# Performance work log

Hardware: AMD Instinct MI355X
Metric: run time of the kernel (lower is better)

Reference implementation:

```python
import jax, jax.numpy as jnp
import numpy as np

NMUL = 1
NEARZERO = 1e-5
ROUTING_LEN = 15
N_DYN = 3
N_STATIC = 13  # layout includes parRT, parAC (present in STATIC_PARAM_NAMES but unused in the step)


def _descale(x, lb, ub):
    return lb + x * (ub - lb)


def setup_inputs() -> dict:
    key = jax.random.key(0)
    k1, k2, k3 = jax.random.split(key, 3)
    T, G = 365, 50000
    u = jax.random.uniform(k1, (T, G, 3), dtype=jnp.float32)
    prcp = u[..., 0] * 10.0                 # mm/day
    tmean = (u[..., 1] - 0.3) * 20.0        # degC, roughly [-6, 14] so snow branch is exercised
    pet = u[..., 2] * 5.0                   # mm/day
    forcing = jnp.stack([prcp, tmean, pet], axis=-1)
    dyn_raw = jax.random.uniform(k2, (T, G, N_DYN * NMUL), dtype=jnp.float32)
    static_raw = jax.random.uniform(k3, (G, N_STATIC * NMUL + 2), dtype=jnp.float32)
    return {"forcing": forcing, "dyn_raw": dyn_raw, "static_raw": static_raw}


def _hbv_forward(forcing, dyn_raw, static_raw):
    T, G, _ = forcing.shape
    dt = forcing.dtype
    # --- descale dynamic params (per-timestep): parBETA, parK0, parBETAET ---
    dyn = dyn_raw.reshape(T, G, N_DYN, NMUL)
    parBETA = _descale(dyn[:, :, 0], 1.0, 6.0)
    parK0 = _descale(dyn[:, :, 1], 0.05, 0.9)
    parBETAET = _descale(dyn[:, :, 2], 0.3, 5.0)
    # --- descale static params ---
    st = static_raw[:, :N_STATIC * NMUL].reshape(G, N_STATIC, NMUL)
    parFC = _descale(st[:, 0], 50.0, 1000.0)
    parK1 = _descale(st[:, 1], 0.01, 0.5)
    parK2 = _descale(st[:, 2], 0.001, 0.2)
    parLP = _descale(st[:, 3], 0.2, 1.0)
    parPERC = _descale(st[:, 4], 0.0, 10.0)
    parUZL = _descale(st[:, 5], 0.0, 100.0)
    parTT = _descale(st[:, 6], -2.5, 2.5)
    parCFMAX = _descale(st[:, 7], 0.5, 10.0)
    parCFR = _descale(st[:, 8], 0.0, 0.1)
    parCWH = _descale(st[:, 9], 0.0, 0.2)
    parC = _descale(st[:, 10], 0.0, 1.0)
    rout = static_raw[:, N_STATIC * NMUL:]
    rout_a = _descale(rout[:, 0], 0.0, 2.9)
    rout_b = _descale(rout[:, 1], 0.0, 6.5)

    Pm = jnp.broadcast_to(forcing[..., 0:1], (T, G, NMUL))
    Tm = jnp.broadcast_to(forcing[..., 1:2], (T, G, NMUL))
    PETm = jnp.broadcast_to(forcing[..., 2:3], (T, G, NMUL))

    def step(carry, xs):
        SNOWPACK, MELTWATER, SM, SUZ, SLZ = carry
        PRECIP, TEMP, PET, pBETA, pK0, pBETAET = xs
        is_rain = (TEMP >= parTT).astype(dt)
        RAIN = PRECIP * is_rain
        SNOW = PRECIP * (1.0 - is_rain)
        SNOWPACK = SNOWPACK + SNOW
        melt = jnp.minimum(jnp.maximum(parCFMAX * (TEMP - parTT), 0.0), SNOWPACK)
        MELTWATER = MELTWATER + melt
        SNOWPACK = SNOWPACK - melt
        refreezing = jnp.minimum(jnp.maximum(parCFR * parCFMAX * (parTT - TEMP), 0.0), MELTWATER)
        SNOWPACK = SNOWPACK + refreezing
        MELTWATER = MELTWATER - refreezing
        tosoil = jnp.maximum(MELTWATER - parCWH * SNOWPACK, 0.0)
        MELTWATER = MELTWATER - tosoil
        soil_wetness = jnp.clip((SM / parFC) ** pBETA, 0.0, 1.0)
        recharge = (RAIN + tosoil) * soil_wetness
        SM = SM + RAIN + tosoil - recharge
        excess = jnp.maximum(SM - parFC, 0.0)
        SM = SM - excess
        evapfactor = jnp.clip((SM / (parLP * parFC)) ** pBETAET, 0.0, 1.0)
        ETact = jnp.minimum(SM, PET * evapfactor)
        SM = jnp.maximum(SM - ETact, NEARZERO)
        capillary = jnp.minimum(SLZ, parC * SLZ * (1.0 - jnp.minimum(SM / parFC, 1.0)))
        SM = jnp.maximum(SM + capillary, NEARZERO)
        SLZ = jnp.maximum(SLZ - capillary, NEARZERO)
        SUZ = SUZ + recharge + excess
        PERC = jnp.minimum(SUZ, parPERC)
        SUZ = SUZ - PERC
        Q0 = pK0 * jnp.maximum(SUZ - parUZL, 0.0)
        SUZ = SUZ - Q0
        Q1 = parK1 * SUZ
        SUZ = SUZ - Q1
        SLZ = jnp.maximum(SLZ + PERC, 0.0)
        Q2 = parK2 * SLZ
        SLZ = SLZ - Q2
        return (SNOWPACK, MELTWATER, SM, SUZ, SLZ), Q0 + Q1 + Q2

    init = tuple(jnp.full((G, NMUL), 0.001, dtype=dt) for _ in range(5))
    _, Qall = jax.lax.scan(step, init, (Pm, Tm, PETm, parBETA, parK0, parBETAET))
    Qsim = Qall.mean(axis=-1)  # [T, G]: average over nmul components

    # --- gamma unit-hydrograph routing (hydroDL UH_gamma + causal conv, lenF = 15) ---
    aa = jax.nn.relu(rout_a) + 0.1      # shape param, [G]
    theta = jax.nn.relu(rout_b) + 0.5   # scale param, [G]
    t = jnp.arange(0.5, ROUTING_LEN, dtype=dt)[:, None]  # [15, 1] midpoints
    w = (t ** (aa - 1.0)) * jnp.exp(-t / theta) / (jnp.exp(jax.lax.lgamma(aa)) * theta ** aa)
    w = w / w.sum(axis=0)  # [15, G], normalized UH weights
    Qpad = jnp.pad(Qsim, ((ROUTING_LEN - 1, 0), (0, 0)))
    # causal conv: Qrout[t] = sum_k w[k] * Qsim[t-k]; fixed 15-tap loop
    Qrout = sum(w[k] * jax.lax.dynamic_slice_in_dim(Qpad, ROUTING_LEN - 1 - k, T, axis=0)
                for k in range(ROUTING_LEN))
    return Qrout  # streamflow [T, G]


def reference(forcing, dyn_raw, static_raw):
    return _hbv_forward(forcing, dyn_raw, static_raw)
```

## Files before the change

kernel.cpp:

```cpp
#include <hip/hip_runtime.h>

#define NEARZERO 1e-5f
#define RLEN 15
#define LOG2E 1.4426950408889634f

struct __attribute__((packed, aligned(4))) F3 { float x, y, z; };
static __device__ __forceinline__ F3 ld3f(const float* p) {
    return *reinterpret_cast<const F3*>(p);
}

struct Par { float FC, invFC, invLPFC, K1, K2, PERC, UZL, TT, CFMAX, CFRC, CWH, C; };

template<int PH>
__device__ __forceinline__ float one_step(
    const F3& f, const F3& d3, const Par& pr,
    float& SNOWPACK, float& MELTWATER, float& SM, float& SUZ, float& SLZ,
    float (&acc)[RLEN], const float (&w)[RLEN])
{
    const float pBETA   = fmaf(d3.x, 5.0f, 1.0f);
    const float pK0     = fmaf(d3.y, 0.85f, 0.05f);
    const float pBETAET = fmaf(d3.z, 4.7f, 0.3f);

    const float d    = f.y - pr.TT;
    const float RAIN = (d >= 0.0f) ? f.x : 0.0f;
    SNOWPACK += f.x - RAIN;
    const float melt = __builtin_amdgcn_fmed3f(pr.CFMAX * d, 0.0f, SNOWPACK);
    MELTWATER += melt;
    SNOWPACK  -= melt;
    const float refr = __builtin_amdgcn_fmed3f(pr.CFRC * (0.0f - d), 0.0f, MELTWATER);
    SNOWPACK  += refr;
    MELTWATER -= refr;
    const float tosoil = fmaxf(fmaf(-pr.CWH, SNOWPACK, MELTWATER), 0.0f);
    MELTWATER -= tosoil;

    const float sw = fminf(exp2f(pBETA * __log2f(SM * pr.invFC)), 1.0f);
    const float rt = RAIN + tosoil;
    const float recharge = rt * sw;
    SM = SM + rt - recharge;
    const float excess = fmaxf(SM - pr.FC, 0.0f);
    SM -= excess;
    const float ef = fminf(exp2f(pBETAET * __log2f(SM * pr.invLPFC)), 1.0f);
    const float ETact = fminf(SM, f.z * ef);
    SM = fmaxf(SM - ETact, NEARZERO);
    const float capillary = pr.C * SLZ * (1.0f - fminf(SM * pr.invFC, 1.0f));
    SM  = fmaxf(SM + capillary, NEARZERO);
    SLZ = fmaxf(SLZ - capillary, NEARZERO);

    SUZ += recharge + excess;
    const float PERC = fminf(SUZ, pr.PERC);
    SUZ -= PERC;
    const float Q0 = pK0 * fmaxf(SUZ - pr.UZL, 0.0f);
    SUZ -= Q0;
    const float Q1 = pr.K1 * SUZ;
    SUZ -= Q1;
    SLZ += PERC;
    const float Q2 = pr.K2 * SLZ;
    SLZ -= Q2;
    const float Qsim = Q0 + Q1 + Q2;

    const float qr = fmaf(w[0], Qsim, acc[PH]);
    acc[PH] = 0.0f;
#pragma unroll
    for (int k = 1; k < RLEN; ++k) {
        const int j = (PH + k) % RLEN;
        acc[j] = fmaf(w[k], Qsim, acc[j]);
    }
    return qr;
}

__global__ __launch_bounds__(64, 1)
void hbv_kernel(const float* __restrict__ forcing,
                const float* __restrict__ dynr,
                const float* __restrict__ statr,
                float* __restrict__ out,
                int G)
{
    const int lane = threadIdx.x;
    const int g  = blockIdx.x * 64 + lane;
    const int gc = (g < G) ? g : (G - 1);
    const bool guard = (g < G);

    const float* sp = statr + (size_t)gc * 15;
    Par pr;
    pr.FC    = fmaf(sp[0], 950.0f, 50.0f);
    pr.K1    = fmaf(sp[1], 0.49f, 0.01f);
    pr.K2    = fmaf(sp[2], 0.199f, 0.001f);
    const float parLP = fmaf(sp[3], 0.8f, 0.2f);
    pr.PERC  = sp[4] * 10.0f;
    pr.UZL   = sp[5] * 100.0f;
    pr.TT    = fmaf(sp[6], 5.0f, -2.5f);
    pr.CFMAX = fmaf(sp[7], 9.5f, 0.5f);
    pr.CFRC  = (sp[8] * 0.1f) * pr.CFMAX;
    pr.CWH   = sp[9] * 0.2f;
    pr.C     = sp[10];
    const float rout_a = sp[13] * 2.9f;
    const float rout_b = sp[14] * 6.5f;
    pr.invFC   = 1.0f / pr.FC;
    pr.invLPFC = 1.0f / (parLP * pr.FC);

    const float aa    = fmaxf(rout_a, 0.0f) + 0.1f;
    const float theta = fmaxf(rout_b, 0.0f) + 0.5f;
    const float am1   = aa - 1.0f;
    const float nitl2 = -LOG2E / theta;
    float w[RLEN];
    float wsum = 0.0f;
#pragma unroll
    for (int k = 0; k < RLEN; ++k) {
        const float tk = (float)k + 0.5f;
        w[k] = exp2f(am1 * __log2f(tk) + tk * nitl2);
        wsum += w[k];
    }
    const float winv = 1.0f / wsum;
#pragma unroll
    for (int k = 0; k < RLEN; ++k) w[k] *= winv;

    float SP_ = 0.001f, MW = 0.001f, SM = 0.001f, SUZ = 0.001f, SLZ = 0.001f;
    float acc[RLEN];
#pragma unroll
    for (int k = 0; k < RLEN; ++k) acc[k] = 0.0f;

    const size_t sT = (size_t)G * 3;
    const float* pF = forcing + (size_t)gc * 3;
    const float* pD = dynr    + (size_t)gc * 3;

    F3 bF[3], bD[3];
    bF[0] = ld3f(pF);          bD[0] = ld3f(pD);
    bF[1] = ld3f(pF + sT);     bD[1] = ld3f(pD + sT);
    bF[2] = ld3f(pF + 2 * sT); bD[2] = ld3f(pD + 2 * sT);

    const float* rF = pF + 3 * sT;
    const float* rD = pD + 3 * sT;
    float* outp = out + g;

#define STEP(PH, FP, DP) do { \
    constexpr int P_ = (PH) % RLEN; \
    constexpr int S_ = P_ % 3; \
    const float qr_ = one_step<P_>(bF[S_], bD[S_], pr, \
                                   SP_, MW, SM, SUZ, SLZ, acc, w); \
    bF[S_] = ld3f(FP); bD[S_] = ld3f(DP); \
    __builtin_amdgcn_sched_barrier(0x7); \
    if (guard) __builtin_nontemporal_store(qr_, outp); \
    outp += G; \
} while (0)

#define STEPADV(PH) do { \
    STEP(PH, rF, rD); \
    rF += sT; rD += sT; \
} while (0)

    for (int i = 0; i < 24; ++i) {
        STEPADV(0);  STEPADV(1);  STEPADV(2);  STEPADV(3);  STEPADV(4);
        STEPADV(5);  STEPADV(6);  STEPADV(7);  STEPADV(8);  STEPADV(9);
        STEPADV(10); STEPADV(11); STEPADV(12); STEPADV(13); STEPADV(14);
    }
#define TR(T) ((((T) + 3) <= 364) ? ((T) + 3) : 364)
    STEP(0, pF + (size_t)TR(360) * sT, pD + (size_t)TR(360) * sT);
    STEP(1, pF + (size_t)TR(361) * sT, pD + (size_t)TR(361) * sT);
    STEP(2, pF + (size_t)TR(362) * sT, pD + (size_t)TR(362) * sT);
    STEP(3, pF + (size_t)TR(363) * sT, pD + (size_t)TR(363) * sT);
    STEP(4, pF + (size_t)TR(364) * sT, pD + (size_t)TR(364) * sT);
#undef TR
#undef STEPADV
#undef STEP
}

extern "C" void kernel_launch(void* const* d_in, const int* in_sizes, int n_in,
                              void* d_out, int out_size, void* d_ws, size_t ws_size,
                              hipStream_t stream) {
    const float* forcing = (const float*)d_in[0];
    const float* dynr    = (const float*)d_in[1];
    const float* statr   = (const float*)d_in[2];
    float* out = (float*)d_out;

    const int G = in_sizes[2] / 15;
    const int block = 64;
    const int grid  = (G + block - 1) / block;
    hbv_kernel<<<grid, block, 0, stream>>>(forcing, dynr, statr, out, G);
}
```

Baseline: 114.1 us.

## Split HBV step into snow/soil and groundwater/routing halves, software-pipelined

Splits each timestep into a snow/soil phase and a groundwater/routing phase. The soil phase for step t+1 is issued right after the routing phase of step t, and capillary flow uses a precomputed C*SLZ product, so the two dependency chains can overlap. The prefetch depth grows from 3 to 5 timesteps. Output stores go from nontemporal to regular stores. This adds register pressure and a more complex prologue and epilogue, and reassociating SM updates may change rounding slightly.

```diff
diff --git a/kernel.cpp b/kernel.cpp
--- a/kernel.cpp
+++ b/kernel.cpp
@@ -12,60 +12,68 @@
 struct Par { float FC, invFC, invLPFC, K1, K2, PERC, UZL, TT, CFMAX, CFRC, CWH, C; };
 
 template<int PH>
-__device__ __forceinline__ float one_step(
-    const F3& f, const F3& d3, const Par& pr,
-    float& SNOWPACK, float& MELTWATER, float& SM, float& SUZ, float& SLZ,
-    float (&acc)[RLEN], const float (&w)[RLEN])
+__device__ __forceinline__ void finish_step(
+    const Par& pr, float& SUZ, float& SLZ,
+    float rxP, float k0P,
+    float (&acc)[RLEN], const float (&w)[RLEN],
+    float& cs, float*& outp, int G, bool guard)
 {
-    const float pBETA   = fmaf(d3.x, 5.0f, 1.0f);
-    const float pK0     = fmaf(d3.y, 0.85f, 0.05f);
-    const float pBETAET = fmaf(d3.z, 4.7f, 0.3f);
-
-    const float d    = f.y - pr.TT;
-    const float RAIN = (d >= 0.0f) ? f.x : 0.0f;
-    SNOWPACK += f.x - RAIN;
-    const float melt = __builtin_amdgcn_fmed3f(pr.CFMAX * d, 0.0f, SNOWPACK);
-    MELTWATER += melt;
-    SNOWPACK  -= melt;
-    const float refr = __builtin_amdgcn_fmed3f(pr.CFRC * (0.0f - d), 0.0f, MELTWATER);
-    SNOWPACK  += refr;
-    MELTWATER -= refr;
-    const float tosoil = fmaxf(fmaf(-pr.CWH, SNOWPACK, MELTWATER), 0.0f);
-    MELTWATER -= tosoil;
-
-    const float sw = fminf(exp2f(pBETA * __log2f(SM * pr.invFC)), 1.0f);
-    const float rt = RAIN + tosoil;
-    const float recharge = rt * sw;
-    SM = SM + rt - recharge;
-    const float excess = fmaxf(SM - pr.FC, 0.0f);
-    SM -= excess;
-    const float ef = fminf(exp2f(pBETAET * __log2f(SM * pr.invLPFC)), 1.0f);
-    const float ETact = fminf(SM, f.z * ef);
-    SM = fmaxf(SM - ETact, NEARZERO);
-    const float capillary = pr.C * SLZ * (1.0f - fminf(SM * pr.invFC, 1.0f));
-    SM  = fmaxf(SM + capillary, NEARZERO);
-    SLZ = fmaxf(SLZ - capillary, NEARZERO);
-
-    SUZ += recharge + excess;
-    const float PERC = fminf(SUZ, pr.PERC);
-    SUZ -= PERC;
-    const float Q0 = pK0 * fmaxf(SUZ - pr.UZL, 0.0f);
+    SUZ += rxP;
+    const float PERCv = fminf(SUZ, pr.PERC);
+    SUZ -= PERCv;
+    const float Q0 = k0P * fmaxf(SUZ - pr.UZL, 0.0f);
     SUZ -= Q0;
     const float Q1 = pr.K1 * SUZ;
     SUZ -= Q1;
-    SLZ += PERC;
+    SLZ += PERCv;
     const float Q2 = pr.K2 * SLZ;
     SLZ -= Q2;
-    const float Qsim = Q0 + Q1 + Q2;
-
-    const float qr = fmaf(w[0], Qsim, acc[PH]);
+    const float Qs = Q0 + Q1 + Q2;
+
+    const float qr = fmaf(w[0], Qs, acc[PH]);
     acc[PH] = 0.0f;
 #pragma unroll
     for (int k = 1; k < RLEN; ++k) {
         const int j = (PH + k) % RLEN;
-        acc[j] = fmaf(w[k], Qsim, acc[j]);
-    }
-    return qr;
+        acc[j] = fmaf(w[k], Qs, acc[j]);
+    }
+    if (guard) *outp = qr;
+    outp += G;
+    cs = pr.C * SLZ;
+}
+
+__device__ __forceinline__ void ab_step(
+    const F3& f, const F3& d3, const Par& pr,
+    float& SP, float& MW, float& SM, float& SLZ,
+    float cs, float& rxP, float& k0P)
+{
+    const float pBETA   = fmaf(d3.x, 5.0f, 1.0f);
+    const float pBETAET = fmaf(d3.z, 4.7f, 0.3f);
+
+    const float dT   = f.y - pr.TT;
+    const float RAIN = (dT >= 0.0f) ? f.x : 0.0f;
+    SP += f.x - RAIN;
+    const float melt = __builtin_amdgcn_fmed3f(pr.CFMAX * dT, 0.0f, SP);
+    MW += melt;  SP -= melt;
+    const float refr = __builtin_amdgcn_fmed3f(pr.CFRC * (0.0f - dT), 0.0f, MW);
+    SP += refr;  MW -= refr;
+    const float tosoil = fmaxf(fmaf(-pr.CWH, SP, MW), 0.0f);
+    MW -= tosoil;
+
+    const float sw = fminf(exp2f(pBETA * __log2f(SM * pr.invFC)), 1.0f);
+    const float rt = RAIN + tosoil;
+    const float rc = rt * sw;
+    SM = fmaf(rt, 1.0f - sw, SM);
+    const float ex = fmaxf(SM - pr.FC, 0.0f);
+    SM = fminf(SM, pr.FC);
+    const float ef = fminf(exp2f(pBETAET * __log2f(SM * pr.invLPFC)), 1.0f);
+    SM = fmaxf(SM - f.z * ef, NEARZERO);
+    const float cap = cs * (1.0f - fminf(SM * pr.invFC, 1.0f));
+    SM  = fmaxf(SM + cap, NEARZERO);
+    SLZ = fmaxf(SLZ - cap, NEARZERO);
+
+    rxP = rc + ex;
+    k0P = fmaf(d3.y, 0.85f, 0.05f);
 }
 
 __global__ __launch_bounds__(64, 1)
@@ -118,50 +126,66 @@
     float acc[RLEN];
 #pragma unroll
     for (int k = 0; k < RLEN; ++k) acc[k] = 0.0f;
+    float rxP = 0.0f, k0P = 0.0f, cs = 0.0f;
 
     const size_t sT = (size_t)G * 3;
     const float* pF = forcing + (size_t)gc * 3;
     const float* pD = dynr    + (size_t)gc * 3;
-
-    F3 bF[3], bD[3];
+    float* outp = out + g;
+
+    F3 bF[5], bD[5];
     bF[0] = ld3f(pF);          bD[0] = ld3f(pD);
     bF[1] = ld3f(pF + sT);     bD[1] = ld3f(pD + sT);
     bF[2] = ld3f(pF + 2 * sT); bD[2] = ld3f(pD + 2 * sT);
-
-    const float* rF = pF + 3 * sT;
-    const float* rD = pD + 3 * sT;
-    float* outp = out + g;
-
-#define STEP(PH, FP, DP) do { \
-    constexpr int P_ = (PH) % RLEN; \
-    constexpr int S_ = P_ % 3; \
-    const float qr_ = one_step<P_>(bF[S_], bD[S_], pr, \
-                                   SP_, MW, SM, SUZ, SLZ, acc, w); \
+    bF[3] = ld3f(pF + 3 * sT); bD[3] = ld3f(pD + 3 * sT);
+    bF[4] = ld3f(pF + 4 * sT); bD[4] = ld3f(pD + 4 * sT);
+
+    const float* rF = pF + 5 * sT;
+    const float* rD = pD + 5 * sT;
+
+    cs = pr.C * SLZ;
+    {
+        const F3 f_ = bF[0], d_ = bD[0];
+        bF[0] = ld3f(rF); bD[0] = ld3f(rD);
+        rF += sT; rD += sT;
+        __builtin_amdgcn_sched_barrier(0x7);
+        ab_step(f_, d_, pr, SP_, MW, SM, SLZ, cs, rxP, k0P);
+    }
+
+#define ITER(MM, FP, DP) do { \
+    constexpr int PH_ = (MM) % RLEN; \
+    constexpr int S_  = ((MM) + 1) % 5; \
+    finish_step<PH_>(pr, SUZ, SLZ, rxP, k0P, acc, w, cs, outp, G, guard); \
+    const F3 f_ = bF[S_], d_ = bD[S_]; \
     bF[S_] = ld3f(FP); bD[S_] = ld3f(DP); \
     __builtin_amdgcn_sched_barrier(0x7); \
-    if (guard) __builtin_nontemporal_store(qr_, outp); \
-    outp += G; \
+    ab_step(f_, d_, pr, SP_, MW, SM, SLZ, cs, rxP, k0P); \
 } while (0)
 
-#define STEPADV(PH) do { \
-    STEP(PH, rF, rD); \
-    rF += sT; rD += sT; \
+#define ITERADV(MM) do { ITER(MM, rF, rD); rF += sT; rD += sT; } while (0)
+
+#define ITER_NL(MM) do { \
+    constexpr int PH_ = (MM) % RLEN; \
+    constexpr int S_  = ((MM) + 1) % 5; \
+    finish_step<PH_>(pr, SUZ, SLZ, rxP, k0P, acc, w, cs, outp, G, guard); \
+    const F3 f_ = bF[S_], d_ = bD[S_]; \
+    ab_step(f_, d_, pr, SP_, MW, SM, SLZ, cs, rxP, k0P); \
 } while (0)
 
-    for (int i = 0; i < 24; ++i) {
-        STEPADV(0);  STEPADV(1);  STEPADV(2);  STEPADV(3);  STEPADV(4);
-        STEPADV(5);  STEPADV(6);  STEPADV(7);  STEPADV(8);  STEPADV(9);
-        STEPADV(10); STEPADV(11); STEPADV(12); STEPADV(13); STEPADV(14);
-    }
-#define TR(T) ((((T) + 3) <= 364) ? ((T) + 3) : 364)
-    STEP(0, pF + (size_t)TR(360) * sT, pD + (size_t)TR(360) * sT);
-    STEP(1, pF + (size_t)TR(361) * sT, pD + (size_t)TR(361) * sT);
-    STEP(2, pF + (size_t)TR(362) * sT, pD + (size_t)TR(362) * sT);
-    STEP(3, pF + (size_t)TR(363) * sT, pD + (size_t)TR(363) * sT);
-    STEP(4, pF + (size_t)TR(364) * sT, pD + (size_t)TR(364) * sT);
-#undef TR
-#undef STEPADV
-#undef STEP
+    for (int i = 0; i < 23; ++i) {
+        ITERADV(0);  ITERADV(1);  ITERADV(2);  ITERADV(3);  ITERADV(4);
+        ITERADV(5);  ITERADV(6);  ITERADV(7);  ITERADV(8);  ITERADV(9);
+        ITERADV(10); ITERADV(11); ITERADV(12); ITERADV(13); ITERADV(14);
+    }
+    ITERADV(0);  ITERADV(1);  ITERADV(2);  ITERADV(3);  ITERADV(4);
+    ITERADV(5);  ITERADV(6);  ITERADV(7);  ITERADV(8);  ITERADV(9);
+    ITERADV(10); ITERADV(11); ITERADV(12); ITERADV(13);
+    ITER(14, pF + (size_t)364 * sT, pD + (size_t)364 * sT);
+    ITER_NL(0); ITER_NL(1); ITER_NL(2); ITER_NL(3);
+    finish_step<4>(pr, SUZ, SLZ, rxP, k0P, acc, w, cs, outp, G, guard);
+#undef ITER_NL
+#undef ITERADV
+#undef ITER
 }
 
 extern "C" void kernel_launch(void* const* d_in, const int* in_sizes, int n_in,
```

New measurement: 103.9 us. 1.1x faster.

## Add producer wave staging inputs to LDS ring and software-pipeline the step

Applied to the files above, without the earlier changes.

Each block now has two waves. One producer wave streams forcing and dynamic parameters into a double-buffered LDS ring ten timesteps at a time, and the consumer wave runs the recurrence from LDS, with __syncthreads handing off between them. The step is also skewed so the groundwater part of step t overlaps the log2 work of step t+1, which shortens the serial dependency chain, and global addressing moves to 32-bit byte offsets. The aim is to hide global load latency behind the serial compute, at the cost of a barrier every group, LDS traffic, and an extra wave per CU slot.

```diff
diff --git a/kernel.cpp b/kernel.cpp
--- a/kernel.cpp
+++ b/kernel.cpp
@@ -3,165 +3,266 @@
 #define NEARZERO 1e-5f
 #define RLEN 15
 #define LOG2E 1.4426950408889634f
+#define GRP 10
 
 struct __attribute__((packed, aligned(4))) F3 { float x, y, z; };
-static __device__ __forceinline__ F3 ld3f(const float* p) {
-    return *reinterpret_cast<const F3*>(p);
+static __device__ __forceinline__ F3 ldo(const char* base, unsigned voff) {
+    return *reinterpret_cast<const F3*>(base + voff);
 }
 
 struct Par { float FC, invFC, invLPFC, K1, K2, PERC, UZL, TT, CFMAX, CFRC, CWH, C; };
 
+struct CState {
+    Par pr;
+    float SP, MW, SM, SUZ, SLZ, rxP, k0P;
+    float acc[RLEN], w[RLEN];
+    char* obase;
+    unsigned vO, G4;
+    bool guard;
+};
+
+__device__ __forceinline__ void ab_step0(CState& st, const F3 f, const F3 d3)
+{
+    const Par& pr = st.pr;
+    const float cs = pr.C * st.SLZ;
+    const float dT   = f.y - pr.TT;
+    const float RAIN = (dT >= 0.0f) ? f.x : 0.0f;
+    st.SP += f.x - RAIN;
+    const float melt = __builtin_amdgcn_fmed3f(pr.CFMAX * dT, 0.0f, st.SP);
+    st.MW += melt;  st.SP -= melt;
+    const float refr = __builtin_amdgcn_fmed3f(pr.CFRC * (0.0f - dT), 0.0f, st.MW);
+    st.SP += refr;  st.MW -= refr;
+    const float tosoil = fmaxf(fmaf(-pr.CWH, st.SP, st.MW), 0.0f);
+    st.MW -= tosoil;
+    const float sw = fminf(exp2f(fmaf(d3.x, 5.0f, 1.0f) * __log2f(st.SM * pr.invFC)), 1.0f);
+    const float rt = RAIN + tosoil;
+    const float rc = rt * sw;
+    st.SM = fmaf(rt, 1.0f - sw, st.SM);
+    const float ex = fmaxf(st.SM - pr.FC, 0.0f);
+    st.SM = fminf(st.SM, pr.FC);
+    const float ef = fminf(exp2f(fmaf(d3.z, 4.7f, 0.3f) * __log2f(st.SM * pr.invLPFC)), 1.0f);
+    st.SM = fmaxf(st.SM - f.z * ef, NEARZERO);
+    const float cap = cs * (1.0f - fminf(st.SM * pr.invFC, 1.0f));
+    st.SM  = fmaxf(st.SM + cap, NEARZERO);
+    st.SLZ = fmaxf(st.SLZ - cap, NEARZERO);
+    st.rxP = rc + ex;
+    st.k0P = fmaf(d3.y, 0.85f, 0.05f);
+}
+
 template<int PH>
-__device__ __forceinline__ float one_step(
-    const F3& f, const F3& d3, const Par& pr,
-    float& SNOWPACK, float& MELTWATER, float& SM, float& SUZ, float& SLZ,
-    float (&acc)[RLEN], const float (&w)[RLEN])
-{
-    const float pBETA   = fmaf(d3.x, 5.0f, 1.0f);
-    const float pK0     = fmaf(d3.y, 0.85f, 0.05f);
-    const float pBETAET = fmaf(d3.z, 4.7f, 0.3f);
-
-    const float d    = f.y - pr.TT;
-    const float RAIN = (d >= 0.0f) ? f.x : 0.0f;
-    SNOWPACK += f.x - RAIN;
-    const float melt = __builtin_amdgcn_fmed3f(pr.CFMAX * d, 0.0f, SNOWPACK);
-    MELTWATER += melt;
-    SNOWPACK  -= melt;
-    const float refr = __builtin_amdgcn_fmed3f(pr.CFRC * (0.0f - d), 0.0f, MELTWATER);
-    SNOWPACK  += refr;
-    MELTWATER -= refr;
-    const float tosoil = fmaxf(fmaf(-pr.CWH, SNOWPACK, MELTWATER), 0.0f);
-    MELTWATER -= tosoil;
-
-    const float sw = fminf(exp2f(pBETA * __log2f(SM * pr.invFC)), 1.0f);
+__device__ __forceinline__ void fused_st(CState& st, const F3 f, const F3 d3)
+{
+    const Par& pr = st.pr;
+    const float t1 = __log2f(st.SM * pr.invFC);
+    const float dT   = f.y - pr.TT;
+    const float RAIN = (dT >= 0.0f) ? f.x : 0.0f;
+    st.SP += f.x - RAIN;
+    const float melt = __builtin_amdgcn_fmed3f(pr.CFMAX * dT, 0.0f, st.SP);
+    st.MW += melt;  st.SP -= melt;
+    const float refr = __builtin_amdgcn_fmed3f(pr.CFRC * (0.0f - dT), 0.0f, st.MW);
+    st.SP += refr;  st.MW -= refr;
+    const float tosoil = fmaxf(fmaf(-pr.CWH, st.SP, st.MW), 0.0f);
+    st.MW -= tosoil;
+    st.SUZ += st.rxP;
+    const float PERCv = fminf(st.SUZ, pr.PERC);
+    st.SUZ -= PERCv;
+    const float Q0 = st.k0P * fmaxf(st.SUZ - pr.UZL, 0.0f);
+    st.SUZ -= Q0;
+    const float Q1 = pr.K1 * st.SUZ;
+    st.SUZ -= Q1;
+    const float sw = fminf(exp2f(fmaf(d3.x, 5.0f, 1.0f) * t1), 1.0f);
     const float rt = RAIN + tosoil;
-    const float recharge = rt * sw;
-    SM = SM + rt - recharge;
-    const float excess = fmaxf(SM - pr.FC, 0.0f);
-    SM -= excess;
-    const float ef = fminf(exp2f(pBETAET * __log2f(SM * pr.invLPFC)), 1.0f);
-    const float ETact = fminf(SM, f.z * ef);
-    SM = fmaxf(SM - ETact, NEARZERO);
-    const float capillary = pr.C * SLZ * (1.0f - fminf(SM * pr.invFC, 1.0f));
-    SM  = fmaxf(SM + capillary, NEARZERO);
-    SLZ = fmaxf(SLZ - capillary, NEARZERO);
-
-    SUZ += recharge + excess;
-    const float PERC = fminf(SUZ, pr.PERC);
-    SUZ -= PERC;
-    const float Q0 = pK0 * fmaxf(SUZ - pr.UZL, 0.0f);
-    SUZ -= Q0;
-    const float Q1 = pr.K1 * SUZ;
-    SUZ -= Q1;
-    SLZ += PERC;
-    const float Q2 = pr.K2 * SLZ;
-    SLZ -= Q2;
-    const float Qsim = Q0 + Q1 + Q2;
-
-    const float qr = fmaf(w[0], Qsim, acc[PH]);
-    acc[PH] = 0.0f;
+    st.SLZ += PERCv;
+    const float Q2 = pr.K2 * st.SLZ;
+    st.SLZ -= Q2;
+    const float Qs = Q0 + Q1 + Q2;
+    const float cs = pr.C * st.SLZ;
+    const float rc = rt * sw;
+    st.SM = fmaf(rt, 1.0f - sw, st.SM);
+    const float ex = fmaxf(st.SM - pr.FC, 0.0f);
+    st.SM = fminf(st.SM, pr.FC);
+    const float t2 = __log2f(st.SM * pr.invLPFC);
+    const float qr = fmaf(st.w[0], Qs, st.acc[PH]);
+    st.acc[PH] = 0.0f;
 #pragma unroll
     for (int k = 1; k < RLEN; ++k) {
         const int j = (PH + k) % RLEN;
-        acc[j] = fmaf(w[k], Qsim, acc[j]);
-    }
-    return qr;
-}
-
-__global__ __launch_bounds__(64, 1)
+        st.acc[j] = fmaf(st.w[k], Qs, st.acc[j]);
+    }
+    if (st.guard) __builtin_nontemporal_store(qr, (float*)(st.obase + st.vO));
+    st.vO += st.G4;
+    const float ef = fminf(exp2f(fmaf(d3.z, 4.7f, 0.3f) * t2), 1.0f);
+    st.SM = fmaxf(st.SM - f.z * ef, NEARZERO);
+    const float cap = cs * (1.0f - fminf(st.SM * pr.invFC, 1.0f));
+    st.SM  = fmaxf(st.SM + cap, NEARZERO);
+    st.SLZ = fmaxf(st.SLZ - cap, NEARZERO);
+    st.rxP = rc + ex;
+    st.k0P = fmaf(d3.y, 0.85f, 0.05f);
+}
+
+template<int PH>
+__device__ __forceinline__ void finish_last(CState& st)
+{
+    const Par& pr = st.pr;
+    st.SUZ += st.rxP;
+    const float PERCv = fminf(st.SUZ, pr.PERC);
+    st.SUZ -= PERCv;
+    const float Q0 = st.k0P * fmaxf(st.SUZ - pr.UZL, 0.0f);
+    st.SUZ -= Q0;
+    const float Q1 = pr.K1 * st.SUZ;
+    st.SUZ -= Q1;
+    st.SLZ += PERCv;
+    const float Q2 = pr.K2 * st.SLZ;
+    st.SLZ -= Q2;
+    const float Qs = Q0 + Q1 + Q2;
+    const float qr = fmaf(st.w[0], Qs, st.acc[PH]);
+    if (st.guard) __builtin_nontemporal_store(qr, (float*)(st.obase + st.vO));
+}
+
+template<int PH0, int CNT, bool FIRST, int I>
+__device__ __forceinline__ void grp_step(const float (*buf)[64][6], int lane, CState& st,
+                                         F3& fA, F3& dA, F3& fB, F3& dB)
+{
+    if constexpr (I + 1 < CNT) {
+        if constexpr (((I + 1) & 1) == 0) {
+            fA = *reinterpret_cast<const F3*>(&buf[I + 1][lane][0]);
+            dA = *reinterpret_cast<const F3*>(&buf[I + 1][lane][3]);
+        } else {
+            fB = *reinterpret_cast<const F3*>(&buf[I + 1][lane][0]);
+            dB = *reinterpret_cast<const F3*>(&buf[I + 1][lane][3]);
+        }
+    }
+    __builtin_amdgcn_sched_barrier(0x7);
+    if constexpr (FIRST && I == 0) {
+        ab_step0(st, fA, dA);
+    } else {
+        constexpr int PH = (PH0 + I) % RLEN;
+        if constexpr ((I & 1) == 0) fused_st<PH>(st, fA, dA);
+        else                        fused_st<PH>(st, fB, dB);
+    }
+    if constexpr (I + 1 < CNT)
+        grp_step<PH0, CNT, FIRST, I + 1>(buf, lane, st, fA, dA, fB, dB);
+}
+
+template<int PH0, int CNT, bool FIRST>
+__device__ __forceinline__ void consume_group(const float (*buf)[64][6], int lane, CState& st)
+{
+    F3 fA, dA, fB, dB;
+    fA = *reinterpret_cast<const F3*>(&buf[0][lane][0]);
+    dA = *reinterpret_cast<const F3*>(&buf[0][lane][3]);
+    fB = fA; dB = dA;
+    grp_step<PH0, CNT, FIRST, 0>(buf, lane, st, fA, dA, fB, dB);
+}
+
+__global__ __launch_bounds__(128, 1)
 void hbv_kernel(const float* __restrict__ forcing,
                 const float* __restrict__ dynr,
                 const float* __restrict__ statr,
                 float* __restrict__ out,
                 int G)
 {
-    const int lane = threadIdx.x;
+    __shared__ float ring[2][GRP][64][6];
+
+    const int lane = threadIdx.x & 63;
+    const int wave = threadIdx.x >> 6;
     const int g  = blockIdx.x * 64 + lane;
     const int gc = (g < G) ? g : (G - 1);
-    const bool guard = (g < G);
-
-    const float* sp = statr + (size_t)gc * 15;
-    Par pr;
-    pr.FC    = fmaf(sp[0], 950.0f, 50.0f);
-    pr.K1    = fmaf(sp[1], 0.49f, 0.01f);
-    pr.K2    = fmaf(sp[2], 0.199f, 0.001f);
-    const float parLP = fmaf(sp[3], 0.8f, 0.2f);
-    pr.PERC  = sp[4] * 10.0f;
-    pr.UZL   = sp[5] * 100.0f;
-    pr.TT    = fmaf(sp[6], 5.0f, -2.5f);
-    pr.CFMAX = fmaf(sp[7], 9.5f, 0.5f);
-    pr.CFRC  = (sp[8] * 0.1f) * pr.CFMAX;
-    pr.CWH   = sp[9] * 0.2f;
-    pr.C     = sp[10];
-    const float rout_a = sp[13] * 2.9f;
-    const float rout_b = sp[14] * 6.5f;
-    pr.invFC   = 1.0f / pr.FC;
-    pr.invLPFC = 1.0f / (parLP * pr.FC);
-
-    const float aa    = fmaxf(rout_a, 0.0f) + 0.1f;
-    const float theta = fmaxf(rout_b, 0.0f) + 0.5f;
-    const float am1   = aa - 1.0f;
-    const float nitl2 = -LOG2E / theta;
-    float w[RLEN];
-    float wsum = 0.0f;
-#pragma unroll
-    for (int k = 0; k < RLEN; ++k) {
-        const float tk = (float)k + 0.5f;
-        w[k] = exp2f(am1 * __log2f(tk) + tk * nitl2);
-        wsum += w[k];
-    }
-    const float winv = 1.0f / wsum;
-#pragma unroll
-    for (int k = 0; k < RLEN; ++k) w[k] *= winv;
-
-    float SP_ = 0.001f, MW = 0.001f, SM = 0.001f, SUZ = 0.001f, SLZ = 0.001f;
-    float acc[RLEN];
-#pragma unroll
-    for (int k = 0; k < RLEN; ++k) acc[k] = 0.0f;
-
-    const size_t sT = (size_t)G * 3;
-    const float* pF = forcing + (size_t)gc * 3;
-    const float* pD = dynr    + (size_t)gc * 3;
-
-    F3 bF[3], bD[3];
-    bF[0] = ld3f(pF);          bD[0] = ld3f(pD);
-    bF[1] = ld3f(pF + sT);     bD[1] = ld3f(pD + sT);
-    bF[2] = ld3f(pF + 2 * sT); bD[2] = ld3f(pD + 2 * sT);
-
-    const float* rF = pF + 3 * sT;
-    const float* rD = pD + 3 * sT;
-    float* outp = out + g;
-
-#define STEP(PH, FP, DP) do { \
-    constexpr int P_ = (PH) % RLEN; \
-    constexpr int S_ = P_ % 3; \
-    const float qr_ = one_step<P_>(bF[S_], bD[S_], pr, \
-                                   SP_, MW, SM, SUZ, SLZ, acc, w); \
-    bF[S_] = ld3f(FP); bD[S_] = ld3f(DP); \
-    __builtin_amdgcn_sched_barrier(0x7); \
-    if (guard) __builtin_nontemporal_store(qr_, outp); \
-    outp += G; \
-} while (0)
-
-#define STEPADV(PH) do { \
-    STEP(PH, rF, rD); \
-    rF += sT; rD += sT; \
-} while (0)
-
-    for (int i = 0; i < 24; ++i) {
-        STEPADV(0);  STEPADV(1);  STEPADV(2);  STEPADV(3);  STEPADV(4);
-        STEPADV(5);  STEPADV(6);  STEPADV(7);  STEPADV(8);  STEPADV(9);
-        STEPADV(10); STEPADV(11); STEPADV(12); STEPADV(13); STEPADV(14);
-    }
-#define TR(T) ((((T) + 3) <= 364) ? ((T) + 3) : 364)
-    STEP(0, pF + (size_t)TR(360) * sT, pD + (size_t)TR(360) * sT);
-    STEP(1, pF + (size_t)TR(361) * sT, pD + (size_t)TR(361) * sT);
-    STEP(2, pF + (size_t)TR(362) * sT, pD + (size_t)TR(362) * sT);
-    STEP(3, pF + (size_t)TR(363) * sT, pD + (size_t)TR(363) * sT);
-    STEP(4, pF + (size_t)TR(364) * sT, pD + (size_t)TR(364) * sT);
-#undef TR
-#undef STEPADV
-#undef STEP
+
+    const char* fbase = (const char*)forcing;
+    const char* dbase = (const char*)dynr;
+    const unsigned G12 = (unsigned)G * 12u;
+
+    if (wave == 0) {
+        unsigned vP = (unsigned)gc * 12u;
+        F3 A0[5], B0_[5], A1[5], B1_[5];
+#define LOAD5(X, Y) do { _Pragma("unroll") \
+        for (int r = 0; r < 5; ++r) { X[r] = ldo(fbase, vP); Y[r] = ldo(dbase, vP); vP += G12; } } while (0)
+#define WR5(BP, S0, X, Y) do { _Pragma("unroll") \
+        for (int r = 0; r < 5; ++r) { \
+            *reinterpret_cast<F3*>(&(BP)[(S0) + r][lane][0]) = X[r]; \
+            *reinterpret_cast<F3*>(&(BP)[(S0) + r][lane][3]) = Y[r]; } } while (0)
+#define STAGE10(BI) do { float (*bp_)[64][6] = ring[BI]; \
+        LOAD5(A0, B0_); LOAD5(A1, B1_); \
+        WR5(bp_, 0, A0, B0_); WR5(bp_, 5, A1, B1_); } while (0)
+
+        STAGE10(0);
+        __syncthreads();
+        for (int k = 1; k <= 35; ++k) {
+            STAGE10(k & 1);
+            __syncthreads();
+        }
+        {
+            float (*bp_)[64][6] = ring[0];
+            LOAD5(A0, B0_);
+            WR5(bp_, 0, A0, B0_);
+        }
+        __syncthreads();
+        return;
+#undef STAGE10
+#undef WR5
+#undef LOAD5
+    }
+
+    CState st;
+    {
+        const float* sp = statr + (size_t)gc * 15;
+        st.pr.FC    = fmaf(sp[0], 950.0f, 50.0f);
+        st.pr.K1    = fmaf(sp[1], 0.49f, 0.01f);
+        st.pr.K2    = fmaf(sp[2], 0.199f, 0.001f);
+        const float parLP = fmaf(sp[3], 0.8f, 0.2f);
+        st.pr.PERC  = sp[4] * 10.0f;
+        st.pr.UZL   = sp[5] * 100.0f;
+        st.pr.TT    = fmaf(sp[6], 5.0f, -2.5f);
+        st.pr.CFMAX = fmaf(sp[7], 9.5f, 0.5f);
+        st.pr.CFRC  = (sp[8] * 0.1f) * st.pr.CFMAX;
+        st.pr.CWH   = sp[9] * 0.2f;
+        st.pr.C     = sp[10];
+        const float rout_a = sp[13] * 2.9f;
+        const float rout_b = sp[14] * 6.5f;
+        st.pr.invFC   = 1.0f / st.pr.FC;
+        st.pr.invLPFC = 1.0f / (parLP * st.pr.FC);
+
+        const float aa    = fmaxf(rout_a, 0.0f) + 0.1f;
+        const float theta = fmaxf(rout_b, 0.0f) + 0.5f;
+        const float am1   = aa - 1.0f;
+        const float nitl2 = -LOG2E / theta;
+        float wsum = 0.0f;
+#pragma unroll
+        for (int k = 0; k < RLEN; ++k) {
+            const float tk = (float)k + 0.5f;
+            st.w[k] = exp2f(am1 * __log2f(tk) + tk * nitl2);
+            wsum += st.w[k];
+        }
+        const float winv = 1.0f / wsum;
+#pragma unroll
+        for (int k = 0; k < RLEN; ++k) st.w[k] *= winv;
+
+        st.SP = 0.001f; st.MW = 0.001f; st.SM = 0.001f; st.SUZ = 0.001f; st.SLZ = 0.001f;
+#pragma unroll
+        for (int k = 0; k < RLEN; ++k) st.acc[k] = 0.0f;
+        st.rxP = 0.0f; st.k0P = 0.0f;
+        st.obase = (char*)out;
+        st.vO = (unsigned)g * 4u;
+        st.G4 = (unsigned)G * 4u;
+        st.guard = (g < G);
+    }
+
+    const float (*r0)[64][6] = (const float (*)[64][6])ring[0];
+    const float (*r1)[64][6] = (const float (*)[64][6])ring[1];
+
+    __syncthreads();
+    consume_group<14, GRP, true>(r0, lane, st);
+    __syncthreads();
+    for (int k = 1; k <= 35; ++k) {
+        const float (*bp)[64][6] = (k & 1) ? r1 : r0;
+        const int f3 = k % 3;
+        if (f3 == 1)      consume_group<9,  GRP, false>(bp, lane, st);
+        else if (f3 == 2) consume_group<4,  GRP, false>(bp, lane, st);
+        else              consume_group<14, GRP, false>(bp, lane, st);
+        __syncthreads();
+    }
+    consume_group<14, 5, false>(r0, lane, st);
+    finish_last<4>(st);
 }
 
 extern "C" void kernel_launch(void* const* d_in, const int* in_sizes, int n_in,
@@ -173,7 +274,7 @@
     float* out = (float*)d_out;
 
     const int G = in_sizes[2] / 15;
-    const int block = 64;
-    const int grid  = (G + block - 1) / block;
+    const int block = 128;
+    const int grid  = (G + 63) / 64;
     hbv_kernel<<<grid, block, 0, stream>>>(forcing, dynr, statr, out, G);
 }
```

New measurement: 112.4 us. About the same (-1.5%).
